# Kernel optimization log

Hardware: AMD Instinct MI355X
Metric: run time of the kernel (lower is better)

The kernel has to match this reference:

```python
import jax, jax.numpy as jnp
import numpy as np

N_NODES = 50000
N_EDGES = 800000
D_IN = 512
D_OUT = 512


def setup_inputs() -> dict:
    key = jax.random.key(0)
    k1, k2, k3, k4, k5 = jax.random.split(key, 5)
    x = jax.random.normal(k1, (N_NODES, D_IN), dtype=jnp.float32)
    # DGL GraphConv weight: [in_feats, out_feats], xavier-ish scale
    weight = jax.random.normal(k2, (D_IN, D_OUT), dtype=jnp.float32) * (1.0 / np.sqrt(D_IN))
    bias = jax.random.normal(k3, (D_OUT,), dtype=jnp.float32) * 0.01
    src = jax.random.randint(k4, (N_EDGES,), 0, N_NODES, dtype=jnp.int64)
    dst = jax.random.randint(k5, (N_EDGES,), 0, N_NODES, dtype=jnp.int64)
    return {"x": x, "weight": weight, "bias": bias, "src": src, "dst": dst}


def reference(x, weight, bias, src, dst):
    # DGL GraphConv with norm='none': sum messages from src -> dst, then linear.
    # (in_feats == out_feats so DGL aggregates first, then applies W; math is
    # identical either way.)
    msgs = x[src]                                            # [E, D_IN] gather
    agg = jax.ops.segment_sum(msgs, dst, num_segments=N_NODES)  # [N, D_IN]
    return agg @ weight + bias                               # [N, D_OUT]
```

## Files before the change

kernel.cpp:

```cpp
#include <hip/hip_runtime.h>
#include <hip/hip_bf16.h>

#define NN 50000
#define NE 800000
#define DD 512
#define NPAD 50048
#define STRIDE 96

typedef __attribute__((ext_vector_type(8))) short bf16x8;
typedef __attribute__((ext_vector_type(4))) float f32x4;
typedef __attribute__((ext_vector_type(8))) unsigned short u16x8;

__device__ __align__(16) unsigned short g_Wt[DD * DD];
__device__ __align__(16) unsigned short g_xb[(size_t)NN * DD];
__device__ __align__(16) unsigned short g_agg[(size_t)NPAD * DD];
__device__ unsigned g_cnt[NN];
__device__ int g_eidx[(size_t)NN * STRIDE];

static __device__ __forceinline__ unsigned short f2bf(float f) {
    unsigned u = __float_as_uint(f);
    u += 0x7fff + ((u >> 16) & 1);
    return (unsigned short)(u >> 16);
}
static __device__ __forceinline__ float bf2f(unsigned short u) {
    return __uint_as_float((unsigned)u << 16);
}

#define FB_FILL 3125
#define FB_CONV (FB_FILL + 12500)
#define FB_WT   (FB_CONV + 1024)
#define FB_END  (FB_WT + 12)

__global__ void prep_all(const float* __restrict__ x, const float* __restrict__ W,
                         const int* __restrict__ src, const int* __restrict__ dst) {
    int b = blockIdx.x;
    int tid = threadIdx.x;
    if (b < FB_FILL) {
        int i = b * 256 + tid;
        int d = dst[i];
        unsigned pos = atomicAdd(&g_cnt[d], 1u);
        if (pos < STRIDE) g_eidx[(size_t)d * STRIDE + pos] = src[i];
    } else if (b < FB_CONV) {
        size_t base = ((size_t)(b - FB_FILL) * 256 + tid) * 8;
        f32x4 v0 = __builtin_nontemporal_load((const f32x4*)(x + base));
        f32x4 v1 = __builtin_nontemporal_load((const f32x4*)(x + base) + 1);
        u16x8 o;
        o[0] = f2bf(v0[0]); o[1] = f2bf(v0[1]); o[2] = f2bf(v0[2]); o[3] = f2bf(v0[3]);
        o[4] = f2bf(v1[0]); o[5] = f2bf(v1[1]); o[6] = f2bf(v1[2]); o[7] = f2bf(v1[3]);
        *(u16x8*)(g_xb + base) = o;
    } else if (b < FB_WT) {
        int idx = (b - FB_CONV) * 256 + tid;
        int k = idx >> 9, n = idx & 511;
        g_Wt[n * DD + k] = f2bf(W[idx]);
    } else {
        int i = (b - FB_WT) * 256 + tid;
        u16x8 z = {0, 0, 0, 0, 0, 0, 0, 0};
        *(u16x8*)(g_agg + (size_t)NN * DD + (size_t)i * 8) = z;
    }
}

__global__ void aggregate() {
    int v = (blockIdx.x * blockDim.x + threadIdx.x) >> 6;
    int lane = threadIdx.x & 63;
    if (v >= NN) return;
    int deg = (int)g_cnt[v];
    if (deg > STRIDE) deg = STRIDE;
    const int* seg = g_eidx + (size_t)v * STRIDE;
    float a[8] = {0.f, 0.f, 0.f, 0.f, 0.f, 0.f, 0.f, 0.f};
    int i = 0;
    for (; i + 3 < deg; i += 4) {
        int s0 = seg[i], s1 = seg[i + 1], s2 = seg[i + 2], s3 = seg[i + 3];
        int4 q0 = *((const int4*)(g_xb + ((size_t)s0 << 9)) + lane);
        int4 q1 = *((const int4*)(g_xb + ((size_t)s1 << 9)) + lane);
        int4 q2 = *((const int4*)(g_xb + ((size_t)s2 << 9)) + lane);
        int4 q3 = *((const int4*)(g_xb + ((size_t)s3 << 9)) + lane);
        const unsigned short* u0 = (const unsigned short*)&q0;
        const unsigned short* u1 = (const unsigned short*)&q1;
        const unsigned short* u2 = (const unsigned short*)&q2;
        const unsigned short* u3 = (const unsigned short*)&q3;
#pragma unroll
        for (int j = 0; j < 8; ++j)
            a[j] += (bf2f(u0[j]) + bf2f(u1[j])) + (bf2f(u2[j]) + bf2f(u3[j]));
    }
    for (; i + 1 < deg; i += 2) {
        int s0 = seg[i], s1 = seg[i + 1];
        int4 q0 = *((const int4*)(g_xb + ((size_t)s0 << 9)) + lane);
        int4 q1 = *((const int4*)(g_xb + ((size_t)s1 << 9)) + lane);
        const unsigned short* u0 = (const unsigned short*)&q0;
        const unsigned short* u1 = (const unsigned short*)&q1;
#pragma unroll
        for (int j = 0; j < 8; ++j) a[j] += bf2f(u0[j]) + bf2f(u1[j]);
    }
    if (i < deg) {
        int s0 = seg[i];
        int4 q0 = *((const int4*)(g_xb + ((size_t)s0 << 9)) + lane);
        const unsigned short* u0 = (const unsigned short*)&q0;
#pragma unroll
        for (int j = 0; j < 8; ++j) a[j] += bf2f(u0[j]);
    }
    u16x8 o;
#pragma unroll
    for (int j = 0; j < 8; ++j) o[j] = f2bf(a[j]);
    *(u16x8*)(g_agg + ((size_t)v << 9) + lane * 8) = o;
}

#define BM 128
#define BN 256
#define BK 32
#define NWG ((NPAD / BM) * (DD / BN))

__global__ __launch_bounds__(512) void gemm_kernel(float* __restrict__ out,
                                                   const float* __restrict__ bias) {
    __shared__ __align__(16) unsigned short As[BM * BK];
    __shared__ __align__(16) unsigned short Bs[BN * BK];

    {
        int gid = blockIdx.x * 512 + threadIdx.x;
        if (gid < NN) g_cnt[gid] = 0;
    }

    const int q = NWG >> 3, r = NWG & 7;
    int xcd = blockIdx.x & 7, sub = blockIdx.x >> 3;
    int swz = (xcd < r) ? xcd * (q + 1) + sub : r * (q + 1) + (xcd - r) * q + sub;
    const int m0 = (swz >> 1) * BM;
    const int n0 = (swz & 1) * BN;

    const int tid = threadIdx.x;
    const int wave = tid >> 6, lane = tid & 63;
    const int wm = wave >> 2, wn = wave & 3;
    const int quad = lane >> 4, l16 = lane & 15;

    const int srow = lane >> 2;
    const int skoff = (lane & 3) * 8;

    f32x4 acc[4][4];
#pragma unroll
    for (int i = 0; i < 4; ++i)
#pragma unroll
        for (int j = 0; j < 4; ++j) acc[i][j] = (f32x4){0.f, 0.f, 0.f, 0.f};

    const unsigned short* gA = g_agg + (size_t)m0 * DD;
    const unsigned short* gB = g_Wt + (size_t)n0 * DD;

    for (int k0 = 0; k0 < DD; k0 += BK) {
#pragma unroll
        for (int i = 0; i < 3; ++i) {
            int c = wave * 3 + i;
            if (c < 8) {
                __builtin_amdgcn_global_load_lds(
                    (const __attribute__((address_space(1))) void*)
                        (gA + (size_t)(c * 16 + srow) * DD + k0 + skoff),
                    (__attribute__((address_space(3))) void*)(As + c * 512), 16, 0, 0);
            } else {
                __builtin_amdgcn_global_load_lds(
                    (const __attribute__((address_space(1))) void*)
                        (gB + (size_t)((c - 8) * 16 + srow) * DD + k0 + skoff),
                    (__attribute__((address_space(3))) void*)(Bs + (c - 8) * 512), 16, 0, 0);
            }
        }
        __syncthreads();

        bf16x8 af[4], bf[4];
#pragma unroll
        for (int t = 0; t < 4; ++t) {
            af[t] = *(const bf16x8*)(&As[(wm * 64 + t * 16 + l16) * BK + quad * 8]);
            bf[t] = *(const bf16x8*)(&Bs[(wn * 64 + t * 16 + l16) * BK + quad * 8]);
        }
#pragma unroll
        for (int am = 0; am < 4; ++am)
#pragma unroll
            for (int bn = 0; bn < 4; ++bn)
                acc[am][bn] = __builtin_amdgcn_mfma_f32_16x16x32_bf16(
                    af[am], bf[bn], acc[am][bn], 0, 0, 0);
        __syncthreads();
    }

#pragma unroll
    for (int am = 0; am < 4; ++am) {
        int row_base = m0 + wm * 64 + am * 16 + quad * 4;
#pragma unroll
        for (int bn = 0; bn < 4; ++bn) {
            int col = n0 + wn * 64 + bn * 16 + l16;
            float bv = bias[col];
#pragma unroll
            for (int rr = 0; rr < 4; ++rr) {
                int rowi = row_base + rr;
                if (rowi < NN) out[(size_t)rowi * DD + col] = acc[am][bn][rr] + bv;
            }
        }
    }
}

extern "C" void kernel_launch(void* const* d_in, const int* in_sizes, int n_in,
                              void* d_out, int out_size, void* d_ws, size_t ws_size,
                              hipStream_t stream) {
    const float* x    = (const float*)d_in[0];
    const float* W    = (const float*)d_in[1];
    const float* bias = (const float*)d_in[2];
    const int*   src  = (const int*)d_in[3];
    const int*   dst  = (const int*)d_in[4];
    float* out = (float*)d_out;
    (void)d_ws; (void)ws_size;

    prep_all<<<FB_END, 256, 0, stream>>>(x, W, src, dst);
    aggregate<<<(NN * 64 + 255) / 256, 256, 0, stream>>>();
    gemm_kernel<<<NWG, 512, 0, stream>>>(out, bias);
}
```

Baseline: 403.2 us.

## Fuse neighbor aggregation into GEMM via LDS-resident aggregated tiles

Merges the aggregate and GEMM kernels into one. Each block gathers and sums neighbor rows for 32 nodes at a time straight into LDS, then multiplies that tile against the whole weight matrix and writes the output. This removes the global aggregated buffer, its zero-padding and one kernel launch. In exchange, only 391 blocks run, so fewer waves are available to hide gather latency. Gather and MFMA phases are serialized within each block, and the full weight matrix is reloaded from L2 for every 32-row quarter.

Result: slower. 507.8 us (+25.9%).

```diff
diff --git a/kernel.cpp b/kernel.cpp
--- a/kernel.cpp
+++ b/kernel.cpp
@@ -4,8 +4,9 @@
 #define NN 50000
 #define NE 800000
 #define DD 512
-#define NPAD 50048
 #define STRIDE 96
+#define NBLK 391
+#define LDA_A 520
 
 typedef __attribute__((ext_vector_type(8))) short bf16x8;
 typedef __attribute__((ext_vector_type(4))) float f32x4;
@@ -13,7 +14,6 @@
 
 __device__ __align__(16) unsigned short g_Wt[DD * DD];
 __device__ __align__(16) unsigned short g_xb[(size_t)NN * DD];
-__device__ __align__(16) unsigned short g_agg[(size_t)NPAD * DD];
 __device__ unsigned g_cnt[NN];
 __device__ int g_eidx[(size_t)NN * STRIDE];
 
@@ -29,7 +29,6 @@
 #define FB_FILL 3125
 #define FB_CONV (FB_FILL + 12500)
 #define FB_WT   (FB_CONV + 1024)
-#define FB_END  (FB_WT + 12)
 
 __global__ void prep_all(const float* __restrict__ x, const float* __restrict__ W,
                          const int* __restrict__ src, const int* __restrict__ dst) {
@@ -48,146 +47,120 @@
         o[0] = f2bf(v0[0]); o[1] = f2bf(v0[1]); o[2] = f2bf(v0[2]); o[3] = f2bf(v0[3]);
         o[4] = f2bf(v1[0]); o[5] = f2bf(v1[1]); o[6] = f2bf(v1[2]); o[7] = f2bf(v1[3]);
         *(u16x8*)(g_xb + base) = o;
-    } else if (b < FB_WT) {
+    } else {
         int idx = (b - FB_CONV) * 256 + tid;
         int k = idx >> 9, n = idx & 511;
         g_Wt[n * DD + k] = f2bf(W[idx]);
-    } else {
-        int i = (b - FB_WT) * 256 + tid;
-        u16x8 z = {0, 0, 0, 0, 0, 0, 0, 0};
-        *(u16x8*)(g_agg + (size_t)NN * DD + (size_t)i * 8) = z;
     }
 }
 
-__global__ void aggregate() {
-    int v = (blockIdx.x * blockDim.x + threadIdx.x) >> 6;
-    int lane = threadIdx.x & 63;
-    if (v >= NN) return;
-    int deg = (int)g_cnt[v];
-    if (deg > STRIDE) deg = STRIDE;
-    const int* seg = g_eidx + (size_t)v * STRIDE;
-    float a[8] = {0.f, 0.f, 0.f, 0.f, 0.f, 0.f, 0.f, 0.f};
-    int i = 0;
-    for (; i + 3 < deg; i += 4) {
-        int s0 = seg[i], s1 = seg[i + 1], s2 = seg[i + 2], s3 = seg[i + 3];
-        int4 q0 = *((const int4*)(g_xb + ((size_t)s0 << 9)) + lane);
-        int4 q1 = *((const int4*)(g_xb + ((size_t)s1 << 9)) + lane);
-        int4 q2 = *((const int4*)(g_xb + ((size_t)s2 << 9)) + lane);
-        int4 q3 = *((const int4*)(g_xb + ((size_t)s3 << 9)) + lane);
-        const unsigned short* u0 = (const unsigned short*)&q0;
-        const unsigned short* u1 = (const unsigned short*)&q1;
-        const unsigned short* u2 = (const unsigned short*)&q2;
-        const unsigned short* u3 = (const unsigned short*)&q3;
-#pragma unroll
-        for (int j = 0; j < 8; ++j)
-            a[j] += (bf2f(u0[j]) + bf2f(u1[j])) + (bf2f(u2[j]) + bf2f(u3[j]));
-    }
-    for (; i + 1 < deg; i += 2) {
-        int s0 = seg[i], s1 = seg[i + 1];
-        int4 q0 = *((const int4*)(g_xb + ((size_t)s0 << 9)) + lane);
-        int4 q1 = *((const int4*)(g_xb + ((size_t)s1 << 9)) + lane);
-        const unsigned short* u0 = (const unsigned short*)&q0;
-        const unsigned short* u1 = (const unsigned short*)&q1;
-#pragma unroll
-        for (int j = 0; j < 8; ++j) a[j] += bf2f(u0[j]) + bf2f(u1[j]);
-    }
-    if (i < deg) {
-        int s0 = seg[i];
-        int4 q0 = *((const int4*)(g_xb + ((size_t)s0 << 9)) + lane);
-        const unsigned short* u0 = (const unsigned short*)&q0;
-#pragma unroll
-        for (int j = 0; j < 8; ++j) a[j] += bf2f(u0[j]);
-    }
-    u16x8 o;
-#pragma unroll
-    for (int j = 0; j < 8; ++j) o[j] = f2bf(a[j]);
-    *(u16x8*)(g_agg + ((size_t)v << 9) + lane * 8) = o;
-}
-
-#define BM 128
-#define BN 256
-#define BK 32
-#define NWG ((NPAD / BM) * (DD / BN))
-
-__global__ __launch_bounds__(512) void gemm_kernel(float* __restrict__ out,
-                                                   const float* __restrict__ bias) {
-    __shared__ __align__(16) unsigned short As[BM * BK];
-    __shared__ __align__(16) unsigned short Bs[BN * BK];
-
-    {
-        int gid = blockIdx.x * 512 + threadIdx.x;
-        if (gid < NN) g_cnt[gid] = 0;
-    }
-
-    const int q = NWG >> 3, r = NWG & 7;
-    int xcd = blockIdx.x & 7, sub = blockIdx.x >> 3;
-    int swz = (xcd < r) ? xcd * (q + 1) + sub : r * (q + 1) + (xcd - r) * q + sub;
-    const int m0 = (swz >> 1) * BM;
-    const int n0 = (swz & 1) * BN;
-
+__global__ __launch_bounds__(512) void agg_gemm(float* __restrict__ out,
+                                                const float* __restrict__ bias) {
+    __shared__ __align__(16) unsigned short As[32 * LDA_A];
+    __shared__ __align__(16) unsigned short Bs[512 * 32];
+    const int m_base = blockIdx.x * 128;
     const int tid = threadIdx.x;
     const int wave = tid >> 6, lane = tid & 63;
-    const int wm = wave >> 2, wn = wave & 3;
     const int quad = lane >> 4, l16 = lane & 15;
 
-    const int srow = lane >> 2;
-    const int skoff = (lane & 3) * 8;
+    for (int qtr = 0; qtr < 4; ++qtr) {
+        const int r0 = m_base + qtr * 32;
+        for (int nn = 0; nn < 4; ++nn) {
+            const int lrow = wave * 4 + nn;
+            const int v = r0 + lrow;
+            float a[8] = {0.f, 0.f, 0.f, 0.f, 0.f, 0.f, 0.f, 0.f};
+            if (v < NN) {
+                int deg = (int)g_cnt[v];
+                if (deg > STRIDE) deg = STRIDE;
+                const int* seg = g_eidx + (size_t)v * STRIDE;
+                int i = 0;
+                for (; i + 3 < deg; i += 4) {
+                    int s0 = seg[i], s1 = seg[i + 1], s2 = seg[i + 2], s3 = seg[i + 3];
+                    int4 q0 = *((const int4*)(g_xb + ((size_t)s0 << 9)) + lane);
+                    int4 q1 = *((const int4*)(g_xb + ((size_t)s1 << 9)) + lane);
+                    int4 q2 = *((const int4*)(g_xb + ((size_t)s2 << 9)) + lane);
+                    int4 q3 = *((const int4*)(g_xb + ((size_t)s3 << 9)) + lane);
+                    const unsigned short* u0 = (const unsigned short*)&q0;
+                    const unsigned short* u1 = (const unsigned short*)&q1;
+                    const unsigned short* u2 = (const unsigned short*)&q2;
+                    const unsigned short* u3 = (const unsigned short*)&q3;
+#pragma unroll
+                    for (int j = 0; j < 8; ++j)
+                        a[j] += (bf2f(u0[j]) + bf2f(u1[j])) + (bf2f(u2[j]) + bf2f(u3[j]));
+                }
+                for (; i + 1 < deg; i += 2) {
+                    int s0 = seg[i], s1 = seg[i + 1];
+                    int4 q0 = *((const int4*)(g_xb + ((size_t)s0 << 9)) + lane);
+                    int4 q1 = *((const int4*)(g_xb + ((size_t)s1 << 9)) + lane);
+                    const unsigned short* u0 = (const unsigned short*)&q0;
+                    const unsigned short* u1 = (const unsigned short*)&q1;
+#pragma unroll
+                    for (int j = 0; j < 8; ++j) a[j] += bf2f(u0[j]) + bf2f(u1[j]);
+                }
+                if (i < deg) {
+                    int s0 = seg[i];
+                    int4 q0 = *((const int4*)(g_xb + ((size_t)s0 << 9)) + lane);
+                    const unsigned short* u0 = (const unsigned short*)&q0;
+#pragma unroll
+                    for (int j = 0; j < 8; ++j) a[j] += bf2f(u0[j]);
+                }
+            }
+            u16x8 o;
+#pragma unroll
+            for (int j = 0; j < 8; ++j) o[j] = f2bf(a[j]);
+            *(u16x8*)(&As[lrow * LDA_A + lane * 8]) = o;
+        }
+        f32x4 acc[2][4];
+#pragma unroll
+        for (int m = 0; m < 2; ++m)
+#pragma unroll
+            for (int g = 0; g < 4; ++g) acc[m][g] = (f32x4){0.f, 0.f, 0.f, 0.f};
 
-    f32x4 acc[4][4];
+        for (int k0 = 0; k0 < DD; k0 += 32) {
 #pragma unroll
-    for (int i = 0; i < 4; ++i)
-#pragma unroll
-        for (int j = 0; j < 4; ++j) acc[i][j] = (f32x4){0.f, 0.f, 0.f, 0.f};
-
-    const unsigned short* gA = g_agg + (size_t)m0 * DD;
-    const unsigned short* gB = g_Wt + (size_t)n0 * DD;
-
-    for (int k0 = 0; k0 < DD; k0 += BK) {
-#pragma unroll
-        for (int i = 0; i < 3; ++i) {
-            int c = wave * 3 + i;
-            if (c < 8) {
+            for (int i = 0; i < 4; ++i) {
+                int c = i * 512 + tid;
+                int n = c >> 2;
+                int koff = (c & 3) * 8;
                 __builtin_amdgcn_global_load_lds(
                     (const __attribute__((address_space(1))) void*)
-                        (gA + (size_t)(c * 16 + srow) * DD + k0 + skoff),
-                    (__attribute__((address_space(3))) void*)(As + c * 512), 16, 0, 0);
-            } else {
-                __builtin_amdgcn_global_load_lds(
-                    (const __attribute__((address_space(1))) void*)
-                        (gB + (size_t)((c - 8) * 16 + srow) * DD + k0 + skoff),
-                    (__attribute__((address_space(3))) void*)(Bs + (c - 8) * 512), 16, 0, 0);
+                        (g_Wt + (size_t)n * DD + k0 + koff),
+                    (__attribute__((address_space(3))) void*)(Bs + (size_t)c * 8), 16, 0, 0);
+            }
+            __syncthreads();
+
+            bf16x8 af[2], bf[4];
+            af[0] = *(const bf16x8*)(&As[l16 * LDA_A + k0 + quad * 8]);
+            af[1] = *(const bf16x8*)(&As[(16 + l16) * LDA_A + k0 + quad * 8]);
+#pragma unroll
+            for (int g = 0; g < 4; ++g)
+                bf[g] = *(const bf16x8*)(&Bs[(wave * 64 + g * 16 + l16) * 32 + quad * 8]);
+#pragma unroll
+            for (int m = 0; m < 2; ++m)
+#pragma unroll
+                for (int g = 0; g < 4; ++g)
+                    acc[m][g] = __builtin_amdgcn_mfma_f32_16x16x32_bf16(
+                        af[m], bf[g], acc[m][g], 0, 0, 0);
+            __syncthreads();
+        }
+#pragma unroll
+        for (int m = 0; m < 2; ++m) {
+            int row_base = r0 + m * 16 + quad * 4;
+#pragma unroll
+            for (int g = 0; g < 4; ++g) {
+                int col = wave * 64 + g * 16 + l16;
+                float bv = bias[col];
+#pragma unroll
+                for (int rr = 0; rr < 4; ++rr) {
+                    int row = row_base + rr;
+                    if (row < NN) out[(size_t)row * DD + col] = acc[m][g][rr] + bv;
+                }
             }
         }
-        __syncthreads();
-
-        bf16x8 af[4], bf[4];
-#pragma unroll
-        for (int t = 0; t < 4; ++t) {
-            af[t] = *(const bf16x8*)(&As[(wm * 64 + t * 16 + l16) * BK + quad * 8]);
-            bf[t] = *(const bf16x8*)(&Bs[(wn * 64 + t * 16 + l16) * BK + quad * 8]);
-        }
-#pragma unroll
-        for (int am = 0; am < 4; ++am)
-#pragma unroll
-            for (int bn = 0; bn < 4; ++bn)
-                acc[am][bn] = __builtin_amdgcn_mfma_f32_16x16x32_bf16(
-                    af[am], bf[bn], acc[am][bn], 0, 0, 0);
-        __syncthreads();
     }
-
-#pragma unroll
-    for (int am = 0; am < 4; ++am) {
-        int row_base = m0 + wm * 64 + am * 16 + quad * 4;
-#pragma unroll
-        for (int bn = 0; bn < 4; ++bn) {
-            int col = n0 + wn * 64 + bn * 16 + l16;
-            float bv = bias[col];
-#pragma unroll
-            for (int rr = 0; rr < 4; ++rr) {
-                int rowi = row_base + rr;
-                if (rowi < NN) out[(size_t)rowi * DD + col] = acc[am][bn][rr] + bv;
-            }
-        }
+    if (tid < 128) {
+        int v = m_base + tid;
+        if (v < NN) g_cnt[v] = 0;
     }
 }
 
@@ -202,7 +175,6 @@
     float* out = (float*)d_out;
     (void)d_ws; (void)ws_size;
 
-    prep_all<<<FB_END, 256, 0, stream>>>(x, W, src, dst);
-    aggregate<<<(NN * 64 + 255) / 256, 256, 0, stream>>>();
-    gemm_kernel<<<NWG, 512, 0, stream>>>(out, bias);
+    prep_all<<<FB_WT, 256, 0, stream>>>(x, W, src, dst);
+    agg_gemm<<<NBLK, 512, 0, stream>>>(out, bias);
 }
```
